# Performance work log

Hardware: AMD Instinct MI355X
Metric: run time of the kernel (lower is better)

The kernel has to match this reference:

```python
import jax, jax.numpy as jnp
import numpy as np

B, S, H = 32, 512, 256
MAX_MEL = 2000  # init kwarg max_mel_len
DUR_MAX = 8


def setup_inputs() -> dict:
    key = jax.random.key(0)
    k1, k2 = jax.random.split(key)
    x = jax.random.normal(k1, (B, S, H), dtype=jnp.float32)
    duration = jax.random.randint(k2, (B, S), 0, DUR_MAX, dtype=jnp.int32)
    return {"x": x, "duration": duration, "max_len": MAX_MEL}


def reference(x, duration, max_len):
    # x: [B, S, H]; duration: [B, S] int; max_len unused (kept for API parity).
    batch, seq_len, hidden = x.shape
    max_mel = MAX_MEL

    cumsum = jnp.cumsum(duration, axis=1)            # [B, S]
    pos = jnp.arange(max_mel, dtype=cumsum.dtype)    # [T]

    # Original builds mask = (pos < cumsum[:, :, None]) and takes argmax over S
    # (index of first True), falling back to seq_len-1 when no True, then clamps.
    # That is exactly searchsorted(cumsum, pos, side='right') clipped to S-1:
    # first j with cumsum[j] > pos; returns S (-> clipped to S-1) when pos >= total.
    idx = jax.vmap(lambda c: jnp.searchsorted(c, pos, side='right'))(cumsum)  # [B, T]
    idx = jnp.clip(idx, 0, seq_len - 1)

    output = jnp.take_along_axis(x, idx[:, :, None], axis=1)  # [B, T, H]

    mel_len = jnp.clip(jnp.sum(duration, axis=1), None, max_mel).astype(jnp.int32)  # [B]
    return output, mel_len
```

## Files before the change

kernel.cpp:

```cpp
#include <hip/hip_runtime.h>

constexpr int B_ = 32;
constexpr int S_ = 512;
constexpr int H_ = 256;
constexpr int T_ = 2000;
constexpr int TPB_CHUNK = 32;

__global__ __launch_bounds__(S_) void cumsum_kernel(
    const int* __restrict__ dur,
    const int* __restrict__ max_len_p,
    int* __restrict__ cum,
    float* __restrict__ mel_len_out)
{
    const int b = blockIdx.x;
    const int tid = threadIdx.x;
    __shared__ int s[S_];
    s[tid] = dur[b * S_ + tid];
    __syncthreads();
#pragma unroll
    for (int off = 1; off < S_; off <<= 1) {
        int v = (tid >= off) ? s[tid - off] : 0;
        __syncthreads();
        s[tid] += v;
        __syncthreads();
    }
    cum[b * S_ + tid] = s[tid];
    if (tid == S_ - 1) {
        int total = s[S_ - 1];
        int ml = max_len_p[0];
        mel_len_out[b] = (float)(total < ml ? total : ml);
    }
}

__global__ __launch_bounds__(256) void regulate_kernel(
    const float* __restrict__ x,
    const int* __restrict__ cum,
    float* __restrict__ out)
{
    const int b = blockIdx.y;
    const int tid = threadIdx.x;
    const int wave = tid >> 6;
    const int lane = tid & 63;

    __shared__ int s_cum[S_];
    s_cum[tid] = cum[b * S_ + tid];
    s_cum[tid + 256] = cum[b * S_ + tid + 256];
    __syncthreads();

    const float4* __restrict__ x_b = (const float4*)(x + (size_t)b * S_ * H_);
    float4* __restrict__ out_b = (float4*)(out + (size_t)b * T_ * H_);

    const int t0 = blockIdx.x * TPB_CHUNK;
#pragma unroll
    for (int i = 0; i < TPB_CHUNK / 4; ++i) {
        const int t = t0 + i * 4 + wave;
        if (t < T_) {
            int lo = 0, hi = S_;
            while (lo < hi) {
                int mid = (lo + hi) >> 1;
                if (s_cum[mid] <= t) lo = mid + 1;
                else hi = mid;
            }
            const int idx = lo < (S_ - 1) ? lo : (S_ - 1);
            out_b[(size_t)t * (H_ / 4) + lane] = x_b[(size_t)idx * (H_ / 4) + lane];
        }
    }
}

extern "C" void kernel_launch(void* const* d_in, const int* in_sizes, int n_in,
                              void* d_out, int out_size, void* d_ws, size_t ws_size,
                              hipStream_t stream) {
    const float* x = (const float*)d_in[0];
    const int* duration = (const int*)d_in[1];
    const int* max_len_p = (const int*)d_in[2];

    float* out = (float*)d_out;
    float* mel_len_out = out + (size_t)B_ * T_ * H_;
    int* cum = (int*)d_ws;

    cumsum_kernel<<<B_, S_, 0, stream>>>(duration, max_len_p, cum, mel_len_out);

    dim3 grid((T_ + TPB_CHUNK - 1) / TPB_CHUNK, B_);
    regulate_kernel<<<grid, 256, 0, stream>>>(x, cum, out);
}
```

Before: 92.60 us.

## Scatter index map in prefix-sum kernel, gather with XCD-aware mapping and nontemporal stores

The prefix-sum kernel now writes a full per-frame source index map by scattering each token's index over its duration span, and fills the tail past the total with the last token. That replaces the per-frame binary search in the gather kernel. The gather kernel becomes one frame per wave with a flat grid, remaps blocks so each batch's blocks share an XCD, and uses nontemporal stores for the large output. The cost is a serial scatter loop per thread and an extra workspace round trip for the index array.

```diff
diff --git a/kernel.cpp b/kernel.cpp
--- a/kernel.cpp
+++ b/kernel.cpp
@@ -4,12 +4,14 @@
 constexpr int S_ = 512;
 constexpr int H_ = 256;
 constexpr int T_ = 2000;
-constexpr int TPB_CHUNK = 32;
+constexpr int F4_PER_ROW = H_ / 4;
 
-__global__ __launch_bounds__(S_) void cumsum_kernel(
+typedef float f32x4 __attribute__((ext_vector_type(4)));
+
+__global__ __launch_bounds__(S_) void build_idx_kernel(
     const int* __restrict__ dur,
     const int* __restrict__ max_len_p,
-    int* __restrict__ cum,
+    int* __restrict__ idx,
     float* __restrict__ mel_len_out)
 {
     const int b = blockIdx.x;
@@ -24,47 +26,41 @@
         s[tid] += v;
         __syncthreads();
     }
-    cum[b * S_ + tid] = s[tid];
-    if (tid == S_ - 1) {
-        int total = s[S_ - 1];
-        int ml = max_len_p[0];
+    const int hi = s[tid];
+    const int lo = tid ? s[tid - 1] : 0;
+    const int total = s[S_ - 1];
+
+    int* __restrict__ idx_b = idx + b * T_;
+    const int hic = hi < T_ ? hi : T_;
+    for (int t = lo; t < hic; ++t) idx_b[t] = tid;
+    for (int t = total + tid; t < T_; t += S_) idx_b[t] = S_ - 1;
+
+    if (tid == 0) {
+        const int ml = max_len_p[0];
         mel_len_out[b] = (float)(total < ml ? total : ml);
     }
 }
 
-__global__ __launch_bounds__(256) void regulate_kernel(
-    const float* __restrict__ x,
-    const int* __restrict__ cum,
-    float* __restrict__ out)
+constexpr int BLOCKS_PER_B = (T_ * F4_PER_ROW) / 256;
+constexpr int NUM_XCD = 8;
+
+__global__ __launch_bounds__(256) void gather_kernel(
+    const f32x4* __restrict__ x,
+    const int* __restrict__ idx,
+    f32x4* __restrict__ out)
 {
-    const int b = blockIdx.y;
-    const int tid = threadIdx.x;
-    const int wave = tid >> 6;
-    const int lane = tid & 63;
+    const int id = blockIdx.x;
+    const int xcd = id & (NUM_XCD - 1);
+    const int j = id >> 3;
+    const int b = xcd + NUM_XCD * (j / BLOCKS_PER_B);
+    const int chunk = j % BLOCKS_PER_B;
 
-    __shared__ int s_cum[S_];
-    s_cum[tid] = cum[b * S_ + tid];
-    s_cum[tid + 256] = cum[b * S_ + tid + 256];
-    __syncthreads();
+    const int t = chunk * 4 + (threadIdx.x >> 6);
+    const int lane = threadIdx.x & 63;
 
-    const float4* __restrict__ x_b = (const float4*)(x + (size_t)b * S_ * H_);
-    float4* __restrict__ out_b = (float4*)(out + (size_t)b * T_ * H_);
-
-    const int t0 = blockIdx.x * TPB_CHUNK;
-#pragma unroll
-    for (int i = 0; i < TPB_CHUNK / 4; ++i) {
-        const int t = t0 + i * 4 + wave;
-        if (t < T_) {
-            int lo = 0, hi = S_;
-            while (lo < hi) {
-                int mid = (lo + hi) >> 1;
-                if (s_cum[mid] <= t) lo = mid + 1;
-                else hi = mid;
-            }
-            const int idx = lo < (S_ - 1) ? lo : (S_ - 1);
-            out_b[(size_t)t * (H_ / 4) + lane] = x_b[(size_t)idx * (H_ / 4) + lane];
-        }
-    }
+    const int s = idx[b * T_ + t];
+    const f32x4 v = x[((size_t)b * S_ + s) * F4_PER_ROW + lane];
+    __builtin_nontemporal_store(v, &out[((size_t)b * T_ + t) * F4_PER_ROW + lane]);
 }
 
 extern "C" void kernel_launch(void* const* d_in, const int* in_sizes, int n_in,
@@ -76,10 +72,10 @@
 
     float* out = (float*)d_out;
     float* mel_len_out = out + (size_t)B_ * T_ * H_;
-    int* cum = (int*)d_ws;
+    int* idx = (int*)d_ws;
 
-    cumsum_kernel<<<B_, S_, 0, stream>>>(duration, max_len_p, cum, mel_len_out);
+    build_idx_kernel<<<B_, S_, 0, stream>>>(duration, max_len_p, idx, mel_len_out);
 
-    dim3 grid((T_ + TPB_CHUNK - 1) / TPB_CHUNK, B_);
-    regulate_kernel<<<grid, 256, 0, stream>>>(x, cum, out);
+    gather_kernel<<<B_ * BLOCKS_PER_B, 256, 0, stream>>>(
+        (const f32x4*)x, idx, (f32x4*)out);
 }
```

Result: no change. 91.21 us (-1.5%).

## Fuse cumsum into gather kernel with wave-shuffle scan and nontemporal stores

Applied to the files above, without the earlier changes.

Drops the separate cumsum kernel. Each gather block now recomputes the per-batch prefix sum itself, using a wave-level shuffle scan over paired durations plus a small cross-wave combine in shared memory. This removes one kernel launch and the workspace round trip. The binary search is also unrolled to a fixed 9 steps, and output rows are written with nontemporal stores to avoid polluting the cache. The cost is that the scan is repeated redundantly in every one of the 63 blocks per batch row.

```diff
diff --git a/kernel.cpp b/kernel.cpp
--- a/kernel.cpp
+++ b/kernel.cpp
@@ -4,65 +4,68 @@
 constexpr int S_ = 512;
 constexpr int H_ = 256;
 constexpr int T_ = 2000;
-constexpr int TPB_CHUNK = 32;
+constexpr int F4 = H_ / 4;
+constexpr int ROWS_PER_BLOCK = 32;
+constexpr int NBLK_T = (T_ + ROWS_PER_BLOCK - 1) / ROWS_PER_BLOCK;
 
-__global__ __launch_bounds__(S_) void cumsum_kernel(
+typedef float f32x4 __attribute__((ext_vector_type(4)));
+
+__global__ __launch_bounds__(256) void lenreg_fused_kernel(
+    const f32x4* __restrict__ x,
     const int* __restrict__ dur,
     const int* __restrict__ max_len_p,
-    int* __restrict__ cum,
+    f32x4* __restrict__ out,
     float* __restrict__ mel_len_out)
-{
-    const int b = blockIdx.x;
-    const int tid = threadIdx.x;
-    __shared__ int s[S_];
-    s[tid] = dur[b * S_ + tid];
-    __syncthreads();
-#pragma unroll
-    for (int off = 1; off < S_; off <<= 1) {
-        int v = (tid >= off) ? s[tid - off] : 0;
-        __syncthreads();
-        s[tid] += v;
-        __syncthreads();
-    }
-    cum[b * S_ + tid] = s[tid];
-    if (tid == S_ - 1) {
-        int total = s[S_ - 1];
-        int ml = max_len_p[0];
-        mel_len_out[b] = (float)(total < ml ? total : ml);
-    }
-}
-
-__global__ __launch_bounds__(256) void regulate_kernel(
-    const float* __restrict__ x,
-    const int* __restrict__ cum,
-    float* __restrict__ out)
 {
     const int b = blockIdx.y;
     const int tid = threadIdx.x;
+    const int lane = tid & 63;
     const int wave = tid >> 6;
-    const int lane = tid & 63;
 
     __shared__ int s_cum[S_];
-    s_cum[tid] = cum[b * S_ + tid];
-    s_cum[tid + 256] = cum[b * S_ + tid + 256];
+    __shared__ int s_wsum[4];
+
+    const int2 d2 = ((const int2*)(dur + b * S_))[tid];
+    const int pair = d2.x + d2.y;
+    int scan = pair;
+#pragma unroll
+    for (int off = 1; off < 64; off <<= 1) {
+        const int y = __shfl_up(scan, off);
+        if (lane >= off) scan += y;
+    }
+    if (lane == 63) s_wsum[wave] = scan;
+    __syncthreads();
+    int wprefix = 0;
+#pragma unroll
+    for (int w = 0; w < 4; ++w) wprefix += (w < wave) ? s_wsum[w] : 0;
+    const int excl = wprefix + scan - pair;
+    s_cum[2 * tid]     = excl + d2.x;
+    s_cum[2 * tid + 1] = excl + pair;
     __syncthreads();
 
-    const float4* __restrict__ x_b = (const float4*)(x + (size_t)b * S_ * H_);
-    float4* __restrict__ out_b = (float4*)(out + (size_t)b * T_ * H_);
+    if (blockIdx.x == 0 && tid == 0) {
+        const int total = s_cum[S_ - 1];
+        const int ml = max_len_p[0];
+        mel_len_out[b] = (float)(total < ml ? total : ml);
+    }
 
-    const int t0 = blockIdx.x * TPB_CHUNK;
+    const f32x4* __restrict__ x_b = x + (size_t)b * S_ * F4;
+    f32x4* __restrict__ out_b = out + (size_t)b * T_ * F4;
+
+    const int t0 = blockIdx.x * ROWS_PER_BLOCK;
 #pragma unroll
-    for (int i = 0; i < TPB_CHUNK / 4; ++i) {
+    for (int i = 0; i < ROWS_PER_BLOCK / 4; ++i) {
         const int t = t0 + i * 4 + wave;
         if (t < T_) {
             int lo = 0, hi = S_;
-            while (lo < hi) {
-                int mid = (lo + hi) >> 1;
-                if (s_cum[mid] <= t) lo = mid + 1;
-                else hi = mid;
+#pragma unroll
+            for (int step = 0; step < 9; ++step) {
+                const int mid = (lo + hi) >> 1;
+                if (s_cum[mid] <= t) lo = mid + 1; else hi = mid;
             }
             const int idx = lo < (S_ - 1) ? lo : (S_ - 1);
-            out_b[(size_t)t * (H_ / 4) + lane] = x_b[(size_t)idx * (H_ / 4) + lane];
+            const f32x4 v = x_b[(size_t)idx * F4 + lane];
+            __builtin_nontemporal_store(v, &out_b[(size_t)t * F4 + lane]);
         }
     }
 }
@@ -70,16 +73,14 @@
 extern "C" void kernel_launch(void* const* d_in, const int* in_sizes, int n_in,
                               void* d_out, int out_size, void* d_ws, size_t ws_size,
                               hipStream_t stream) {
-    const float* x = (const float*)d_in[0];
+    const f32x4* x = (const f32x4*)d_in[0];
     const int* duration = (const int*)d_in[1];
     const int* max_len_p = (const int*)d_in[2];
 
     float* out = (float*)d_out;
     float* mel_len_out = out + (size_t)B_ * T_ * H_;
-    int* cum = (int*)d_ws;
 
-    cumsum_kernel<<<B_, S_, 0, stream>>>(duration, max_len_p, cum, mel_len_out);
-
-    dim3 grid((T_ + TPB_CHUNK - 1) / TPB_CHUNK, B_);
-    regulate_kernel<<<grid, 256, 0, stream>>>(x, cum, out);
+    dim3 grid(NBLK_T, B_);
+    lenreg_fused_kernel<<<grid, 256, 0, stream>>>(
+        x, duration, max_len_p, (f32x4*)out, mel_len_out);
 }
```

Measured after the change: 87.96 us. -5.0%, faster.
